# Kernel optimization log

Measured on AMD Instinct MI355X. Metric: run time of the kernel, lower is better.

The kernel has to match this reference:

```python
import jax, jax.numpy as jnp
import numpy as np

B, S, D, H = 4, 2048, 1024, 16
DK = D // H

def setup_inputs() -> dict:
    key = jax.random.key(0)
    ks = jax.random.split(key, 11)
    scale = 1.0 / np.sqrt(D)
    inp = {
        'q': jax.random.normal(ks[0], (B, S, D), jnp.float32),
        'k': jax.random.normal(ks[1], (B, S, D), jnp.float32),
        'v': jax.random.normal(ks[2], (B, S, D), jnp.float32),
        'Wq': jax.random.normal(ks[3], (D, D), jnp.float32) * scale,
        'bq': jnp.zeros((D,), jnp.float32),
        'Wk': jax.random.normal(ks[4], (D, D), jnp.float32) * scale,
        'bk': jnp.zeros((D,), jnp.float32),
        'Wv': jax.random.normal(ks[5], (D, D), jnp.float32) * scale,
        'bv': jnp.zeros((D,), jnp.float32),
        'Wo': jax.random.normal(ks[6], (D, D), jnp.float32) * scale,
        'bo': jnp.zeros((D,), jnp.float32),
        # diagonal mask: 0 on the diagonal (self position masked out), 1 elsewhere
        'mask': (1 - jnp.eye(S, dtype=jnp.int32))[None, None, :, :],
    }
    return inp


def reference(q, k, v, Wq, bq, Wk, bk, Wv, bv, Wo, bo, mask):
    def proj(x, W, b):
        # [B,S,D] -> [B,H,S,DK]
        y = x @ W.T + b
        return y.reshape(B, S, H, DK).transpose(0, 2, 1, 3)

    qh = proj(q, Wq, bq)
    kh = proj(k, Wk, bk)
    vh = proj(v, Wv, bv)

    scores = jnp.einsum('bhsd,bhtd->bhst', qh, kh) / jnp.sqrt(jnp.float32(DK))
    scores = jnp.where(mask == 0, jnp.finfo(scores.dtype).min, scores)
    attn = jax.nn.softmax(scores, axis=-1)  # dropout is identity in eval mode
    out = jnp.einsum('bhst,bhtd->bhsd', attn, vh)
    out = out.transpose(0, 2, 1, 3).reshape(B, S, D)
    return out @ Wo.T + bo
```

## Files before the change

kernel.cpp:

```cpp
#include <hip/hip_runtime.h>
#include <stdint.h>

#define S_LEN 2048
#define D_DIM 1024
#define NB 4
#define NH 16
#define DKH 64
#define M_ROWS (NB * S_LEN)
#define PLD 72

typedef float  f32x4 __attribute__((ext_vector_type(4)));
typedef short  s16x8 __attribute__((ext_vector_type(8)));
typedef unsigned short u16;
typedef u16    u16x4 __attribute__((ext_vector_type(4)));

#define AS1 __attribute__((address_space(1)))
#define AS3 __attribute__((address_space(3)))

__device__ __forceinline__ void gload16(const u16* g, u16* l) {
    __builtin_amdgcn_global_load_lds((const AS1 void*)g, (AS3 void*)l, 16, 0, 0);
}

__device__ __forceinline__ u16 f2bf(float f) {
    uint32_t u = __builtin_bit_cast(uint32_t, f);
    return (u16)((u + 0x7fffu + ((u >> 16) & 1u)) >> 16);
}
__device__ __forceinline__ u16 f2bf_cheap(float f) {
    uint32_t u = __builtin_bit_cast(uint32_t, f);
    return (u16)((u + 0x8000u) >> 16);
}

__global__ __launch_bounds__(256) void conv_kernel(const float* __restrict__ src,
                                                   u16* __restrict__ dst, int n)
{
    int i = (blockIdx.x * 256 + threadIdx.x) * 8;
    if (i + 8 > n) return;
    f32x4 a = *(const f32x4*)(src + i);
    f32x4 b = *(const f32x4*)(src + i + 4);
    s16x8 r;
#pragma unroll
    for (int j = 0; j < 4; ++j) r[j]     = (short)f2bf(a[j]);
#pragma unroll
    for (int j = 0; j < 4; ++j) r[j + 4] = (short)f2bf(b[j]);
    *(s16x8*)(dst + i) = r;
}

__global__ __launch_bounds__(256) void conv3_kernel(const float* __restrict__ a,
                                                    const float* __restrict__ b,
                                                    const float* __restrict__ c,
                                                    u16* __restrict__ dst)
{
    const int z = blockIdx.z;
    const float* src = (z == 0) ? a : (z == 1) ? b : c;
    int i = (blockIdx.x * 256 + threadIdx.x) * 8;
    f32x4 lo = *(const f32x4*)(src + i);
    f32x4 hi = *(const f32x4*)(src + i + 4);
    s16x8 r;
#pragma unroll
    for (int j = 0; j < 4; ++j) r[j]     = (short)f2bf(lo[j]);
#pragma unroll
    for (int j = 0; j < 4; ++j) r[j + 4] = (short)f2bf(hi[j]);
    *(s16x8*)(dst + (size_t)z * (D_DIM * D_DIM) + i) = r;
}

__device__ __forceinline__ void gemm128_body(const u16* __restrict__ X,
                                             const u16* __restrict__ Wt,
                                             int m0, int n0,
                                             u16* As, u16* Bs,
                                             f32x4 acc[4][4])
{
    const int tid  = threadIdx.x;
    const int wv   = tid >> 6;
    const int lane = tid & 63;
    const int ln   = lane & 15;
    const int quad = lane >> 4;
    const int wm   = wv >> 1;
    const int wn   = wv & 1;
    const int l7   = ln & 7;

    for (int k0 = 0; k0 < D_DIM; k0 += 64) {
        __syncthreads();
#pragma unroll
        for (int i = 0; i < 4; ++i) {
            const int c   = tid + i * 256;
            const int row = c >> 3;
            const int sg  = (c & 7) ^ (row & 7);
            const int lb  = (i * 256 + wv * 64) * 8;
            gload16(&X [(size_t)(m0 + row) * D_DIM + k0 + sg * 8], &As[lb]);
            gload16(&Wt[(size_t)(n0 + row) * D_DIM + k0 + sg * 8], &Bs[lb]);
        }
        __syncthreads();
#pragma unroll
        for (int ks = 0; ks < 2; ++ks) {
            const int sA = ((ks * 4 + quad) ^ l7) * 8;
            s16x8 af[4], bfr[4];
#pragma unroll
            for (int t = 0; t < 4; ++t) {
                af[t]  = *(const s16x8*)&As[(wm * 64 + t * 16 + ln) * 64 + sA];
                bfr[t] = *(const s16x8*)&Bs[(wn * 64 + t * 16 + ln) * 64 + sA];
            }
#pragma unroll
            for (int tM = 0; tM < 4; ++tM)
#pragma unroll
                for (int tN = 0; tN < 4; ++tN)
                    acc[tM][tN] = __builtin_amdgcn_mfma_f32_16x16x32_bf16(
                        af[tM], bfr[tN], acc[tM][tN], 0, 0, 0);
        }
    }
}

__global__ __launch_bounds__(256) void qkv128_kernel(
    const u16* __restrict__ xb, const u16* __restrict__ Wb,
    const float* __restrict__ bias, int mode,
    u16* __restrict__ Qh, u16* __restrict__ Kh, u16* __restrict__ Vt)
{
    __shared__ __attribute__((aligned(16))) u16 As[128 * 64];
    __shared__ __attribute__((aligned(16))) u16 Bs[128 * 64];

    const int lin = blockIdx.y * 8 + blockIdx.x;
    const int swz = (lin & 7) * 64 + (lin >> 3);
    const int n0  = (swz & 7) * 128;
    const int m0  = (swz >> 3) * 128;

    f32x4 zero = {0.f, 0.f, 0.f, 0.f};
    f32x4 acc[4][4];
#pragma unroll
    for (int i = 0; i < 4; ++i)
#pragma unroll
        for (int j = 0; j < 4; ++j) acc[i][j] = zero;

    gemm128_body(xb, Wb, m0, n0, As, Bs, acc);

    const int tid  = threadIdx.x;
    const int wv   = tid >> 6;
    const int lane = tid & 63;
    const int ln   = lane & 15;
    const int quad = lane >> 4;
    const int wm   = wv >> 1;
    const int wn   = wv & 1;
    const float qscale = (mode == 0) ? 0.18033688011112042f : 1.0f;

#pragma unroll
    for (int tM = 0; tM < 4; ++tM) {
#pragma unroll
        for (int tN = 0; tN < 4; ++tN) {
            const int ng = n0 + wn * 64 + tN * 16 + ln;
            const float bf32 = bias[ng];
            const int h  = ng >> 6;
            const int dk = ng & 63;
            const int mbase = m0 + wm * 64 + tM * 16 + quad * 4;
            const int b = mbase >> 11;
            const int s = mbase & 2047;
            if (mode == 2) {
                u16x4 pk;
#pragma unroll
                for (int r = 0; r < 4; ++r) pk[r] = f2bf(acc[tM][tN][r] + bf32);
                *(u16x4*)&Vt[((size_t)((b * NH + h) * DKH + dk)) * S_LEN + s] = pk;
            } else {
                u16* dst = (mode == 0) ? Qh : Kh;
#pragma unroll
                for (int r = 0; r < 4; ++r)
                    dst[((size_t)(b * NH + h) * S_LEN + (s + r)) * DKH + dk] =
                        f2bf((acc[tM][tN][r] + bf32) * qscale);
            }
        }
    }
}

__global__ __launch_bounds__(256) void attn_kernel(
    const u16* __restrict__ Qh, const u16* __restrict__ Kh,
    const u16* __restrict__ Vt, u16* __restrict__ ctx)
{
    __shared__ __attribute__((aligned(16))) u16 Ks[64 * 64];
    __shared__ __attribute__((aligned(16))) u16 Vs[64 * 64];
    __shared__ __attribute__((aligned(16))) u16 QPs[64 * PLD];

    const int tid  = threadIdx.x;
    const int wv   = tid >> 6;
    const int lane = tid & 63;
    const int ln   = lane & 15;
    const int quad = lane >> 4;
    const int l7   = ln & 7;

    const int q0 = blockIdx.x * 64;
    const int bh = blockIdx.y;
    const size_t qkbase = (size_t)bh * S_LEN * DKH;
    const size_t vbase  = (size_t)bh * DKH * S_LEN;

#pragma unroll
    for (int i = 0; i < 2; ++i) {
        const int c = tid + i * 256, row = c >> 3;
        const int sg = (c & 7) ^ (row & 7);
        gload16(&Qh[qkbase + (size_t)(q0 + row) * DKH + sg * 8],
                &QPs[(i * 256 + wv * 64) * 8]);
    }
    __syncthreads();

    s16x8 aq[2];
#pragma unroll
    for (int ks = 0; ks < 2; ++ks)
        aq[ks] = *(const s16x8*)&QPs[(wv * 16 + ln) * 64 + (((ks * 4 + quad) ^ l7) * 8)];

    float l_part[4] = {0.f, 0.f, 0.f, 0.f};
    f32x4 zero = {0.f, 0.f, 0.f, 0.f};
    f32x4 o_acc[4] = {zero, zero, zero, zero};

    const int rbase = q0 + wv * 16 + quad * 4;
    const int rowA = wv * 16 + ln;
    const int rotA = (((rowA >> 2) & 7)) * 8;
    const int rotW = ((4 * wv + quad) & 7) * 8;

    for (int kb = 0; kb < S_LEN; kb += 64) {
        __syncthreads();
#pragma unroll
        for (int i = 0; i < 2; ++i) {
            const int c = tid + i * 256, row = c >> 3;
            const int sg = (c & 7) ^ (row & 7);
            const int lb = (i * 256 + wv * 64) * 8;
            gload16(&Kh[qkbase + (size_t)(kb + row) * DKH + sg * 8], &Ks[lb]);
            gload16(&Vt[vbase + (size_t)row * S_LEN + kb + sg * 8], &Vs[lb]);
        }
        __syncthreads();

        f32x4 sf[4];
#pragma unroll
        for (int nt = 0; nt < 4; ++nt) {
            f32x4 acc = zero;
#pragma unroll
            for (int ks = 0; ks < 2; ++ks) {
                s16x8 bk_ = *(const s16x8*)&Ks[(nt * 16 + ln) * 64 + (((ks * 4 + quad) ^ l7) * 8)];
                acc = __builtin_amdgcn_mfma_f32_16x16x32_bf16(aq[ks], bk_, acc, 0, 0, 0);
            }
            sf[nt] = acc;
        }

        if (kb == q0) {
#pragma unroll
            for (int nt = 0; nt < 4; ++nt)
#pragma unroll
                for (int r = 0; r < 4; ++r) {
                    float p = __builtin_amdgcn_exp2f(sf[nt][r]);
                    if (rbase + r == kb + nt * 16 + ln) p = 0.f;
                    sf[nt][r] = p;
                    l_part[r] += p;
                }
        } else {
#pragma unroll
            for (int nt = 0; nt < 4; ++nt)
#pragma unroll
                for (int r = 0; r < 4; ++r) {
                    float p = __builtin_amdgcn_exp2f(sf[nt][r]);
                    sf[nt][r] = p;
                    l_part[r] += p;
                }
        }

#pragma unroll
        for (int nt = 0; nt < 4; ++nt)
#pragma unroll
            for (int r = 0; r < 4; ++r) {
                int row  = wv * 16 + quad * 4 + r;
                int col  = ((nt * 16 + ln) + rotW) & 63;
                QPs[row * PLD + col] = f2bf_cheap(sf[nt][r]);
            }

#pragma unroll
        for (int ks = 0; ks < 2; ++ks) {
            int colA = ((ks * 32 + quad * 8) + rotA) & 63;
            s16x8 ap = *(const s16x8*)&QPs[rowA * PLD + colA];
#pragma unroll
            for (int nt = 0; nt < 4; ++nt) {
                s16x8 bvv = *(const s16x8*)&Vs[(nt * 16 + ln) * 64 + (((ks * 4 + quad) ^ l7) * 8)];
                o_acc[nt] = __builtin_amdgcn_mfma_f32_16x16x32_bf16(ap, bvv, o_acc[nt], 0, 0, 0);
            }
        }
    }

#pragma unroll
    for (int r = 0; r < 4; ++r) {
#pragma unroll
        for (int off = 1; off < 16; off <<= 1)
            l_part[r] += __shfl_xor(l_part[r], off, 16);
    }

    const int b = bh >> 4;
    const int h = bh & 15;
#pragma unroll
    for (int nt = 0; nt < 4; ++nt) {
#pragma unroll
        for (int r = 0; r < 4; ++r) {
            float val = o_acc[nt][r] / l_part[r];
            int sg = q0 + wv * 16 + quad * 4 + r;
            ctx[((size_t)b * S_LEN + sg) * D_DIM + h * DKH + nt * 16 + ln] = f2bf(val);
        }
    }
}

__global__ __launch_bounds__(256) void oproj128_kernel(
    const u16* __restrict__ ctx, const u16* __restrict__ WoB,
    const float* __restrict__ bo, float* __restrict__ out, float sentinel)
{
    __shared__ __attribute__((aligned(16))) u16 As[128 * 64];
    __shared__ __attribute__((aligned(16))) u16 Bs[128 * 64];

    const int lin = blockIdx.y * 8 + blockIdx.x;
    const int swz = (lin & 7) * 64 + (lin >> 3);
    const int n0  = (swz & 7) * 128;
    const int m0  = (swz >> 3) * 128;

    f32x4 zero = {0.f, 0.f, 0.f, 0.f};
    f32x4 acc[4][4];
#pragma unroll
    for (int i = 0; i < 4; ++i)
#pragma unroll
        for (int j = 0; j < 4; ++j) acc[i][j] = zero;

    gemm128_body(ctx, WoB, m0, n0, As, Bs, acc);

    const int tid  = threadIdx.x;
    const int wv   = tid >> 6;
    const int lane = tid & 63;
    const int ln   = lane & 15;
    const int quad = lane >> 4;
    const int wm   = wv >> 1;
    const int wn   = wv & 1;

#pragma unroll
    for (int tM = 0; tM < 4; ++tM) {
#pragma unroll
        for (int tN = 0; tN < 4; ++tN) {
            const int ng = n0 + wn * 64 + tN * 16 + ln;
            const float bf32 = bo[ng];
            const int mbase = m0 + wm * 64 + tM * 16 + quad * 4;
#pragma unroll
            for (int r = 0; r < 4; ++r) {
                float val = acc[tM][tN][r] + bf32;
                if (mbase + r == 0 && ng == 0) val += sentinel;
                out[(size_t)(mbase + r) * D_DIM + ng] = val;
            }
        }
    }
}

extern "C" void kernel_launch(void* const* d_in, const int* in_sizes, int n_in,
                              void* d_out, int out_size, void* d_ws, size_t ws_size,
                              hipStream_t stream)
{
    const float* q  = (const float*)d_in[0];
    const float* k  = (const float*)d_in[1];
    const float* v  = (const float*)d_in[2];
    const float* Wq = (const float*)d_in[3];
    const float* bq = (const float*)d_in[4];
    const float* Wk = (const float*)d_in[5];
    const float* bk = (const float*)d_in[6];
    const float* Wv = (const float*)d_in[7];
    const float* bv = (const float*)d_in[8];
    const float* Wo = (const float*)d_in[9];
    const float* bo = (const float*)d_in[10];

    const size_t headSz = (size_t)NB * NH * S_LEN * DKH;
    u16* Qh  = (u16*)d_ws;
    u16* Kh  = Qh + headSz;
    u16* Vt  = Kh + headSz;
    u16* ctx = Vt + headSz;
    u16* xb  = ctx;
    u16* Wb  = (u16*)d_out;
    u16* WoB = Qh;
    float* out = (float*)d_out;

    float sentinel = 0.f;
    {
        const int expect[12] = {8388608, 8388608, 8388608, 1048576, 1024, 1048576,
                                1024, 1048576, 1024, 1048576, 1024, 4194304};
        bool ok = (n_in == 12);
        for (int i = 0; ok && i < 12; ++i) ok = (in_sizes[i] == expect[i]);
        if (!ok)                               sentinel = 1000.f;
        else if (ws_size < 4 * headSz * 2)     sentinel = 2000.f;
        else if (out_size != (int)headSz)      sentinel = 3000.f;
    }

    const int WN = D_DIM * D_DIM;

    dim3 gw(WN / 2048, 1, 3);
    conv3_kernel<<<gw, 256, 0, stream>>>(Wq, Wk, Wv, Wb);

    dim3 gg(D_DIM / 128, M_ROWS / 128, 1);
    conv_kernel<<<dim3((int)(headSz / 2048)), 256, 0, stream>>>(q, xb, (int)headSz);
    qkv128_kernel<<<gg, 256, 0, stream>>>(xb, Wb + 0 * WN, bq, 0, Qh, Kh, Vt);
    conv_kernel<<<dim3((int)(headSz / 2048)), 256, 0, stream>>>(k, xb, (int)headSz);
    qkv128_kernel<<<gg, 256, 0, stream>>>(xb, Wb + 1 * WN, bk, 1, Qh, Kh, Vt);
    conv_kernel<<<dim3((int)(headSz / 2048)), 256, 0, stream>>>(v, xb, (int)headSz);
    qkv128_kernel<<<gg, 256, 0, stream>>>(xb, Wb + 2 * WN, bv, 2, Qh, Kh, Vt);

    dim3 g2(S_LEN / 64, NB * NH, 1);
    attn_kernel<<<g2, 256, 0, stream>>>(Qh, Kh, Vt, ctx);

    conv_kernel<<<dim3(WN / 2048), 256, 0, stream>>>(Wo, WoB, WN);

    oproj128_kernel<<<gg, 256, 0, stream>>>(ctx, WoB, bo, out, sentinel);
}
```

Before: 390.1 us.

## Double-buffer V/O projection GEMMs, batch Q/K projections, remap attention blocks per XCD

Adds a double-buffered LDS GEMM loop, used by the V projection and the output projection, so the next K-tile is fetched while MFMAs run on the current one. The Q and K projections are merged into one launch with a z dimension, and their input conversions into one conv2 launch; the second converted activation is staged in spare space of the output buffer. The attention grid is remapped so each XCD gets contiguous heads, which should improve L2 reuse of K/V. The cost is doubled LDS per block in the double-buffered kernels, which can lower occupancy, plus more bf16 workspace traffic.

```diff
diff --git a/kernel.cpp b/kernel.cpp
--- a/kernel.cpp
+++ b/kernel.cpp
@@ -45,6 +45,24 @@
     *(s16x8*)(dst + i) = r;
 }
 
+__global__ __launch_bounds__(256) void conv2_kernel(const float* __restrict__ a,
+                                                    const float* __restrict__ b,
+                                                    u16* __restrict__ da,
+                                                    u16* __restrict__ db)
+{
+    const float* src = blockIdx.z ? b : a;
+    u16* dst        = blockIdx.z ? db : da;
+    int i = (blockIdx.x * 256 + threadIdx.x) * 8;
+    f32x4 lo = *(const f32x4*)(src + i);
+    f32x4 hi = *(const f32x4*)(src + i + 4);
+    s16x8 r;
+#pragma unroll
+    for (int j = 0; j < 4; ++j) r[j]     = (short)f2bf(lo[j]);
+#pragma unroll
+    for (int j = 0; j < 4; ++j) r[j + 4] = (short)f2bf(hi[j]);
+    *(s16x8*)(dst + i) = r;
+}
+
 __global__ __launch_bounds__(256) void conv3_kernel(const float* __restrict__ a,
                                                     const float* __restrict__ b,
                                                     const float* __restrict__ c,
@@ -61,6 +79,44 @@
 #pragma unroll
     for (int j = 0; j < 4; ++j) r[j + 4] = (short)f2bf(hi[j]);
     *(s16x8*)(dst + (size_t)z * (D_DIM * D_DIM) + i) = r;
+}
+
+__device__ __forceinline__ void stage_tile(const u16* __restrict__ X,
+                                           const u16* __restrict__ Wt,
+                                           int m0, int n0, int k0,
+                                           u16* As, u16* Bs, int tid, int wv)
+{
+#pragma unroll
+    for (int i = 0; i < 4; ++i) {
+        const int c   = tid + i * 256;
+        const int row = c >> 3;
+        const int sg  = (c & 7) ^ (row & 7);
+        const int lb  = (i * 256 + wv * 64) * 8;
+        gload16(&X [(size_t)(m0 + row) * D_DIM + k0 + sg * 8], &As[lb]);
+        gload16(&Wt[(size_t)(n0 + row) * D_DIM + k0 + sg * 8], &Bs[lb]);
+    }
+}
+
+__device__ __forceinline__ void compute_tile(const u16* As, const u16* Bs,
+                                             f32x4 acc[4][4],
+                                             int wm, int wn, int ln, int quad, int l7)
+{
+#pragma unroll
+    for (int ks = 0; ks < 2; ++ks) {
+        const int sA = ((ks * 4 + quad) ^ l7) * 8;
+        s16x8 af[4], bfr[4];
+#pragma unroll
+        for (int t = 0; t < 4; ++t) {
+            af[t]  = *(const s16x8*)&As[(wm * 64 + t * 16 + ln) * 64 + sA];
+            bfr[t] = *(const s16x8*)&Bs[(wn * 64 + t * 16 + ln) * 64 + sA];
+        }
+#pragma unroll
+        for (int tM = 0; tM < 4; ++tM)
+#pragma unroll
+            for (int tN = 0; tN < 4; ++tN)
+                acc[tM][tN] = __builtin_amdgcn_mfma_f32_16x16x32_bf16(
+                    af[tM], bfr[tN], acc[tM][tN], 0, 0, 0);
+    }
 }
 
 __device__ __forceinline__ void gemm128_body(const u16* __restrict__ X,
@@ -80,57 +136,19 @@
 
     for (int k0 = 0; k0 < D_DIM; k0 += 64) {
         __syncthreads();
-#pragma unroll
-        for (int i = 0; i < 4; ++i) {
-            const int c   = tid + i * 256;
-            const int row = c >> 3;
-            const int sg  = (c & 7) ^ (row & 7);
-            const int lb  = (i * 256 + wv * 64) * 8;
-            gload16(&X [(size_t)(m0 + row) * D_DIM + k0 + sg * 8], &As[lb]);
-            gload16(&Wt[(size_t)(n0 + row) * D_DIM + k0 + sg * 8], &Bs[lb]);
-        }
+        stage_tile(X, Wt, m0, n0, k0, As, Bs, tid, wv);
         __syncthreads();
-#pragma unroll
-        for (int ks = 0; ks < 2; ++ks) {
-            const int sA = ((ks * 4 + quad) ^ l7) * 8;
-            s16x8 af[4], bfr[4];
-#pragma unroll
-            for (int t = 0; t < 4; ++t) {
-                af[t]  = *(const s16x8*)&As[(wm * 64 + t * 16 + ln) * 64 + sA];
-                bfr[t] = *(const s16x8*)&Bs[(wn * 64 + t * 16 + ln) * 64 + sA];
-            }
-#pragma unroll
-            for (int tM = 0; tM < 4; ++tM)
-#pragma unroll
-                for (int tN = 0; tN < 4; ++tN)
-                    acc[tM][tN] = __builtin_amdgcn_mfma_f32_16x16x32_bf16(
-                        af[tM], bfr[tN], acc[tM][tN], 0, 0, 0);
-        }
-    }
-}
-
-__global__ __launch_bounds__(256) void qkv128_kernel(
-    const u16* __restrict__ xb, const u16* __restrict__ Wb,
-    const float* __restrict__ bias, int mode,
-    u16* __restrict__ Qh, u16* __restrict__ Kh, u16* __restrict__ Vt)
-{
-    __shared__ __attribute__((aligned(16))) u16 As[128 * 64];
-    __shared__ __attribute__((aligned(16))) u16 Bs[128 * 64];
-
-    const int lin = blockIdx.y * 8 + blockIdx.x;
-    const int swz = (lin & 7) * 64 + (lin >> 3);
-    const int n0  = (swz & 7) * 128;
-    const int m0  = (swz >> 3) * 128;
-
-    f32x4 zero = {0.f, 0.f, 0.f, 0.f};
-    f32x4 acc[4][4];
-#pragma unroll
-    for (int i = 0; i < 4; ++i)
-#pragma unroll
-        for (int j = 0; j < 4; ++j) acc[i][j] = zero;
-
-    gemm128_body(xb, Wb, m0, n0, As, Bs, acc);
-
+        compute_tile(As, Bs, acc, wm, wn, ln, quad, l7);
+    }
+}
+
+__device__ __forceinline__ void gemm128_dbuf(const u16* __restrict__ X,
+                                             const u16* __restrict__ Wt,
+                                             int m0, int n0,
+                                             u16* As0, u16* Bs0,
+                                             u16* As1, u16* Bs1,
+                                             f32x4 acc[4][4])
+{
     const int tid  = threadIdx.x;
     const int wv   = tid >> 6;
     const int lane = tid & 63;
@@ -138,7 +156,58 @@
     const int quad = lane >> 4;
     const int wm   = wv >> 1;
     const int wn   = wv & 1;
-    const float qscale = (mode == 0) ? 0.18033688011112042f : 1.0f;
+    const int l7   = ln & 7;
+
+    stage_tile(X, Wt, m0, n0, 0, As0, Bs0, tid, wv);
+    __syncthreads();
+    for (int t = 0; t < 16; t += 2) {
+        stage_tile(X, Wt, m0, n0, (t + 1) * 64, As1, Bs1, tid, wv);
+        compute_tile(As0, Bs0, acc, wm, wn, ln, quad, l7);
+        __syncthreads();
+        if (t + 2 < 16)
+            stage_tile(X, Wt, m0, n0, (t + 2) * 64, As0, Bs0, tid, wv);
+        compute_tile(As1, Bs1, acc, wm, wn, ln, quad, l7);
+        __syncthreads();
+    }
+}
+
+__global__ __launch_bounds__(256) void qk_kernel(
+    const u16* __restrict__ xq, const u16* __restrict__ xk,
+    const u16* __restrict__ Wb,
+    const float* __restrict__ bq, const float* __restrict__ bk,
+    u16* __restrict__ Qh, u16* __restrict__ Kh)
+{
+    __shared__ __attribute__((aligned(16))) u16 As[128 * 64];
+    __shared__ __attribute__((aligned(16))) u16 Bs[128 * 64];
+
+    const int mode = blockIdx.z;
+    const u16* X        = mode ? xk : xq;
+    const u16* Wt       = Wb + (size_t)mode * (D_DIM * D_DIM);
+    const float* bias   = mode ? bk : bq;
+    u16* dst            = mode ? Kh : Qh;
+    const float qscale  = mode ? 1.0f : 0.18033688011112042f;
+
+    const int lin = blockIdx.y * 8 + blockIdx.x;
+    const int swz = (lin & 7) * 64 + (lin >> 3);
+    const int n0  = (swz & 7) * 128;
+    const int m0  = (swz >> 3) * 128;
+
+    f32x4 zero = {0.f, 0.f, 0.f, 0.f};
+    f32x4 acc[4][4];
+#pragma unroll
+    for (int i = 0; i < 4; ++i)
+#pragma unroll
+        for (int j = 0; j < 4; ++j) acc[i][j] = zero;
+
+    gemm128_body(X, Wt, m0, n0, As, Bs, acc);
+
+    const int tid  = threadIdx.x;
+    const int wv   = tid >> 6;
+    const int lane = tid & 63;
+    const int ln   = lane & 15;
+    const int quad = lane >> 4;
+    const int wm   = wv >> 1;
+    const int wn   = wv & 1;
 
 #pragma unroll
     for (int tM = 0; tM < 4; ++tM) {
@@ -151,18 +220,60 @@
             const int mbase = m0 + wm * 64 + tM * 16 + quad * 4;
             const int b = mbase >> 11;
             const int s = mbase & 2047;
-            if (mode == 2) {
-                u16x4 pk;
-#pragma unroll
-                for (int r = 0; r < 4; ++r) pk[r] = f2bf(acc[tM][tN][r] + bf32);
-                *(u16x4*)&Vt[((size_t)((b * NH + h) * DKH + dk)) * S_LEN + s] = pk;
-            } else {
-                u16* dst = (mode == 0) ? Qh : Kh;
-#pragma unroll
-                for (int r = 0; r < 4; ++r)
-                    dst[((size_t)(b * NH + h) * S_LEN + (s + r)) * DKH + dk] =
-                        f2bf((acc[tM][tN][r] + bf32) * qscale);
-            }
+#pragma unroll
+            for (int r = 0; r < 4; ++r)
+                dst[((size_t)(b * NH + h) * S_LEN + (s + r)) * DKH + dk] =
+                    f2bf((acc[tM][tN][r] + bf32) * qscale);
+        }
+    }
+}
+
+__global__ __launch_bounds__(256) void vproj_kernel(
+    const u16* __restrict__ xv, const u16* __restrict__ Wv2,
+    const float* __restrict__ bv, u16* __restrict__ Vt)
+{
+    __shared__ __attribute__((aligned(16))) u16 As0[128 * 64];
+    __shared__ __attribute__((aligned(16))) u16 Bs0[128 * 64];
+    __shared__ __attribute__((aligned(16))) u16 As1[128 * 64];
+    __shared__ __attribute__((aligned(16))) u16 Bs1[128 * 64];
+
+    const int lin = blockIdx.y * 8 + blockIdx.x;
+    const int swz = (lin & 7) * 64 + (lin >> 3);
+    const int n0  = (swz & 7) * 128;
+    const int m0  = (swz >> 3) * 128;
+
+    f32x4 zero = {0.f, 0.f, 0.f, 0.f};
+    f32x4 acc[4][4];
+#pragma unroll
+    for (int i = 0; i < 4; ++i)
+#pragma unroll
+        for (int j = 0; j < 4; ++j) acc[i][j] = zero;
+
+    gemm128_dbuf(xv, Wv2, m0, n0, As0, Bs0, As1, Bs1, acc);
+
+    const int tid  = threadIdx.x;
+    const int wv   = tid >> 6;
+    const int lane = tid & 63;
+    const int ln   = lane & 15;
+    const int quad = lane >> 4;
+    const int wm   = wv >> 1;
+    const int wn   = wv & 1;
+
+#pragma unroll
+    for (int tM = 0; tM < 4; ++tM) {
+#pragma unroll
+        for (int tN = 0; tN < 4; ++tN) {
+            const int ng = n0 + wn * 64 + tN * 16 + ln;
+            const float bf32 = bv[ng];
+            const int h  = ng >> 6;
+            const int dk = ng & 63;
+            const int mbase = m0 + wm * 64 + tM * 16 + quad * 4;
+            const int b = mbase >> 11;
+            const int s = mbase & 2047;
+            u16x4 pk;
+#pragma unroll
+            for (int r = 0; r < 4; ++r) pk[r] = f2bf(acc[tM][tN][r] + bf32);
+            *(u16x4*)&Vt[((size_t)((b * NH + h) * DKH + dk)) * S_LEN + s] = pk;
         }
     }
 }
@@ -182,8 +293,12 @@
     const int quad = lane >> 4;
     const int l7   = ln & 7;
 
-    const int q0 = blockIdx.x * 64;
-    const int bh = blockIdx.y;
+    const int lin = blockIdx.y * 32 + blockIdx.x;
+    const int xcd = lin & 7;
+    const int t_  = lin >> 3;
+    const int bh  = xcd * 8 + (t_ >> 5);
+    const int q0  = (t_ & 31) * 64;
+
     const size_t qkbase = (size_t)bh * S_LEN * DKH;
     const size_t vbase  = (size_t)bh * DKH * S_LEN;
 
@@ -300,8 +415,10 @@
     const u16* __restrict__ ctx, const u16* __restrict__ WoB,
     const float* __restrict__ bo, float* __restrict__ out, float sentinel)
 {
-    __shared__ __attribute__((aligned(16))) u16 As[128 * 64];
-    __shared__ __attribute__((aligned(16))) u16 Bs[128 * 64];
+    __shared__ __attribute__((aligned(16))) u16 As0[128 * 64];
+    __shared__ __attribute__((aligned(16))) u16 Bs0[128 * 64];
+    __shared__ __attribute__((aligned(16))) u16 As1[128 * 64];
+    __shared__ __attribute__((aligned(16))) u16 Bs1[128 * 64];
 
     const int lin = blockIdx.y * 8 + blockIdx.x;
     const int swz = (lin & 7) * 64 + (lin >> 3);
@@ -315,7 +432,7 @@
 #pragma unroll
         for (int j = 0; j < 4; ++j) acc[i][j] = zero;
 
-    gemm128_body(ctx, WoB, m0, n0, As, Bs, acc);
+    gemm128_dbuf(ctx, WoB, m0, n0, As0, Bs0, As1, Bs1, acc);
 
     const int tid  = threadIdx.x;
     const int wv   = tid >> 6;
@@ -359,12 +476,13 @@
     const float* bo = (const float*)d_in[10];
 
     const size_t headSz = (size_t)NB * NH * S_LEN * DKH;
+    const int    WN     = D_DIM * D_DIM;
     u16* Qh  = (u16*)d_ws;
     u16* Kh  = Qh + headSz;
     u16* Vt  = Kh + headSz;
     u16* ctx = Vt + headSz;
-    u16* xb  = ctx;
     u16* Wb  = (u16*)d_out;
+    u16* xk  = Wb + 3 * WN;
     u16* WoB = Qh;
     float* out = (float*)d_out;
 
@@ -379,23 +497,17 @@
         else if (out_size != (int)headSz)      sentinel = 3000.f;
     }
 
-    const int WN = D_DIM * D_DIM;
-
-    dim3 gw(WN / 2048, 1, 3);
-    conv3_kernel<<<gw, 256, 0, stream>>>(Wq, Wk, Wv, Wb);
-
-    dim3 gg(D_DIM / 128, M_ROWS / 128, 1);
-    conv_kernel<<<dim3((int)(headSz / 2048)), 256, 0, stream>>>(q, xb, (int)headSz);
-    qkv128_kernel<<<gg, 256, 0, stream>>>(xb, Wb + 0 * WN, bq, 0, Qh, Kh, Vt);
-    conv_kernel<<<dim3((int)(headSz / 2048)), 256, 0, stream>>>(k, xb, (int)headSz);
-    qkv128_kernel<<<gg, 256, 0, stream>>>(xb, Wb + 1 * WN, bk, 1, Qh, Kh, Vt);
-    conv_kernel<<<dim3((int)(headSz / 2048)), 256, 0, stream>>>(v, xb, (int)headSz);
-    qkv128_kernel<<<gg, 256, 0, stream>>>(xb, Wb + 2 * WN, bv, 2, Qh, Kh, Vt);
-
-    dim3 g2(S_LEN / 64, NB * NH, 1);
-    attn_kernel<<<g2, 256, 0, stream>>>(Qh, Kh, Vt, ctx);
+    conv3_kernel<<<dim3(WN / 2048, 1, 3), 256, 0, stream>>>(Wq, Wk, Wv, Wb);
+
+    conv_kernel<<<dim3((int)(headSz / 2048)), 256, 0, stream>>>(v, ctx, (int)headSz);
+    vproj_kernel<<<dim3(8, 64), 256, 0, stream>>>(ctx, Wb + 2 * WN, bv, Vt);
+
+    conv2_kernel<<<dim3((int)(headSz / 2048), 1, 2), 256, 0, stream>>>(q, k, ctx, xk);
+    qk_kernel<<<dim3(8, 64, 2), 256, 0, stream>>>(ctx, xk, Wb, bq, bk, Qh, Kh);
+
+    attn_kernel<<<dim3(S_LEN / 64, NB * NH), 256, 0, stream>>>(Qh, Kh, Vt, ctx);
 
     conv_kernel<<<dim3(WN / 2048), 256, 0, stream>>>(Wo, WoB, WN);
 
-    oproj128_kernel<<<gg, 256, 0, stream>>>(ctx, WoB, bo, out, sentinel);
-}
+    oproj128_kernel<<<dim3(8, 64), 256, 0, stream>>>(ctx, WoB, bo, out, sentinel);
+}
```

New measurement: 386.0 us. About the same (-1.1%).
